# Performance work log

Hardware: AMD Instinct MI355X
Metric: run time of the kernel (lower is better)

Reference implementation:

```python
import jax, jax.numpy as jnp
import numpy as np

N_USERS = 60000
N_ITEMS = 30000
N_NODES = N_USERS + N_ITEMS
D = 64
L = 2


def _norm_adj(edge_index):
    # symmetrize: A_idx = [e, e.flip(0)]
    src = jnp.concatenate([edge_index[0], edge_index[1]])
    dst = jnp.concatenate([edge_index[1], edge_index[0]])
    ones = jnp.ones_like(src, dtype=jnp.float32)
    deg = jax.ops.segment_sum(ones, src, num_segments=N_NODES)
    deg = jnp.clip(deg, 1.0, None)
    val = jax.lax.rsqrt(deg[src]) * jax.lax.rsqrt(deg[dst])
    return src, dst, val


def _spmm(src, dst, val, x):
    # out[i] = sum_{(i,j) in E} val_ij * x[j]
    return jax.ops.segment_sum(val[:, None] * x[dst], src, num_segments=N_NODES)


def setup_inputs() -> dict:
    key = jax.random.key(0)
    ks = jax.random.split(key, 20)
    s = 0.02
    inp = {
        'x_txt': jax.random.normal(ks[0], (N_ITEMS, 768), jnp.float32),
        'x_img': jax.random.normal(ks[1], (N_ITEMS, 512), jnp.float32),
        'x_struct': jax.random.normal(ks[2], (N_ITEMS, 128), jnp.float32),
        'user_emb': jax.random.normal(ks[3], (3, N_USERS, D), jnp.float32) * s,
        'W_txt': jax.random.normal(ks[4], (3, 768, D), jnp.float32) * s,
        'b_txt': jax.random.normal(ks[5], (3, D), jnp.float32) * s,
        'W_img': jax.random.normal(ks[6], (3, 512, D), jnp.float32) * s,
        'b_img': jax.random.normal(ks[7], (3, D), jnp.float32) * s,
        'W_st': jax.random.normal(ks[8], (3, 128, D), jnp.float32) * s,
        'b_st': jax.random.normal(ks[9], (3, D), jnp.float32) * s,
        'Wu1': jax.random.normal(ks[10], (3 * D, 128), jnp.float32) * s,
        'bu1': jax.random.normal(ks[11], (128,), jnp.float32) * s,
        'Wu2': jax.random.normal(ks[12], (128, 3), jnp.float32) * s,
        'bu2': jax.random.normal(ks[13], (3,), jnp.float32) * s,
        'Wi1': jax.random.normal(ks[14], (3 * D, 128), jnp.float32) * s,
        'bi1': jax.random.normal(ks[15], (128,), jnp.float32) * s,
        'Wi2': jax.random.normal(ks[16], (128, 3), jnp.float32) * s,
        'bi2': jax.random.normal(ks[17], (3,), jnp.float32) * s,
        'edge_index': jax.random.randint(ks[18], (2, 500000), 0, N_NODES, jnp.int64),
    }
    return inp


def reference(x_txt, x_img, x_struct, user_emb, W_txt, b_txt, W_img, b_img,
              W_st, b_st, Wu1, bu1, Wu2, bu2, Wi1, bi1, Wi2, bi2, edge_index):
    src, dst, val = _norm_adj(edge_index)

    # item embeddings for all 3 branches at once: [n_items, 3, d]
    i0 = (jnp.einsum('nt,btd->nbd', x_txt, W_txt) + b_txt
          + jnp.einsum('nt,btd->nbd', x_img, W_img) + b_img
          + jnp.einsum('nt,btd->nbd', x_struct, W_st) + b_st)
    u0 = jnp.transpose(user_emb, (1, 0, 2))  # [n_users, 3, d]
    x = jnp.concatenate([u0, i0], axis=0).reshape(N_NODES, 3 * D)

    out = x
    for _ in range(L):
        x = _spmm(src, dst, val, x)
        out = out + x
    out = out / (L + 1)

    stack = out.reshape(N_NODES, 3, D)
    U_stack, I_stack = stack[:N_USERS], stack[N_USERS:]
    U_cat = U_stack.reshape(N_USERS, 3 * D)
    I_cat = I_stack.reshape(N_ITEMS, 3 * D)

    a_u = jax.nn.softmax(jax.nn.relu(U_cat @ Wu1 + bu1) @ Wu2 + bu2, axis=-1)
    a_i = jax.nn.softmax(jax.nn.relu(I_cat @ Wi1 + bi1) @ Wi2 + bi2, axis=-1)

    U = jnp.einsum('nb,nbd->nd', a_u, U_stack)
    I = jnp.einsum('nb,nbd->nd', a_i, I_stack)
    return jnp.concatenate([U, I], axis=0)  # [N_NODES, d]
```

## Files before the change

kernel.cpp:

```cpp
#include <hip/hip_runtime.h>
#include <math.h>

#define N_USERS 60000
#define N_ITEMS 30000
#define N_NODES 90000
#define DD 64
#define FF 192
#define FH 96
#define KK_TOT 1408
#define E_UND 500000
#define E_DIR 1000000
#define SCAN_NBLK 88

typedef __attribute__((ext_vector_type(8))) __bf16 bf16x8;
typedef __attribute__((ext_vector_type(8))) unsigned short u16x8;
typedef __attribute__((ext_vector_type(4))) float f32x4;

__device__ __forceinline__ unsigned short f2bf(float f) {
    unsigned int u = __float_as_uint(f);
    unsigned int r = (u + 0x7FFFu + ((u >> 16) & 1u)) >> 16;
    return (unsigned short)r;
}
__device__ __forceinline__ float bf_lo(unsigned int x) { return __uint_as_float(x << 16); }
__device__ __forceinline__ float bf_hi(unsigned int x) { return __uint_as_float(x & 0xFFFF0000u); }
__device__ __forceinline__ float bf2f(unsigned short x) {
    return __uint_as_float((unsigned int)x << 16);
}
__device__ __forceinline__ unsigned int pack2(float a, float b) {
    return ((unsigned int)f2bf(b) << 16) | (unsigned int)f2bf(a);
}

__global__ void k_mode(const int* __restrict__ ei, int* __restrict__ mode) {
    __shared__ int any;
    if (threadIdx.x == 0) any = 0;
    __syncthreads();
    if (ei[2 * threadIdx.x + 1] != 0) atomicOr(&any, 1);
    __syncthreads();
    if (threadIdx.x == 0) mode[0] = (any == 0) ? 1 : 0;
}

__device__ __forceinline__ void load_pair(const int* __restrict__ ei, int md, int u,
                                          int& a, int& b) {
    if (md) { a = ei[2 * u]; b = ei[2 * (E_UND + u)]; }
    else    { a = ei[u];     b = ei[E_UND + u]; }
}

__global__ void k_deg(const int* __restrict__ ei, const int* __restrict__ mode,
                      int* __restrict__ deg) {
    int i = blockIdx.x * 256 + threadIdx.x;
    if (i >= E_UND) return;
    int md = mode[0];
    int a, b;
    load_pair(ei, md, i, a, b);
    atomicAdd(&deg[a], 1);
    atomicAdd(&deg[b], 1);
}

__global__ __launch_bounds__(1024) void k_scan1(const int* __restrict__ deg,
                                                int* __restrict__ offs,
                                                int* __restrict__ bsum) {
    __shared__ int tmp[1024];
    int b = blockIdx.x, t = threadIdx.x;
    int i = b * 1024 + t;
    int v = (i < N_NODES) ? deg[i] : 0;
    tmp[t] = v;
    __syncthreads();
    for (int off = 1; off < 1024; off <<= 1) {
        int add = (t >= off) ? tmp[t - off] : 0;
        __syncthreads();
        tmp[t] += add;
        __syncthreads();
    }
    offs[i] = tmp[t] - v;
    if (t == 1023) bsum[b] = tmp[t];
}

__global__ void k_scan2(const int* __restrict__ bsum, int* __restrict__ bscan) {
    if (threadIdx.x == 0) {
        int run = 0;
        for (int b = 0; b < SCAN_NBLK; b++) { bscan[b] = run; run += bsum[b]; }
    }
}

__global__ void k_scan3(const int* __restrict__ deg, int* __restrict__ offs,
                        const int* __restrict__ bscan, int* __restrict__ cursor,
                        float* __restrict__ rsq) {
    int i = blockIdx.x * 256 + threadIdx.x;
    if (i >= N_NODES) return;
    int o = offs[i] + bscan[i >> 10];
    offs[i] = o;
    cursor[i] = o;
    int dg = deg[i];
    if (dg < 1) dg = 1;
    rsq[i] = rsqrtf((float)dg);
}

__global__ void k_fill(const int* __restrict__ ei, const int* __restrict__ mode,
                       int* __restrict__ cursor, const float* __restrict__ rsq,
                       int* __restrict__ edst, float* __restrict__ eval) {
    int i = blockIdx.x * 256 + threadIdx.x;
    if (i >= E_DIR) return;
    int md = mode[0];
    int u = (i < E_UND) ? i : i - E_UND;
    int a, b;
    load_pair(ei, md, u, a, b);
    int s, d;
    if (i < E_UND) { s = a; d = b; } else { s = b; d = a; }
    int slot = atomicAdd(&cursor[s], 1);
    edst[slot] = d;
    eval[slot] = rsq[s] * rsq[d];
}

__global__ void k_users(const float* __restrict__ ue, float* __restrict__ S,
                        unsigned short* __restrict__ Xbs) {
    int idx = blockIdx.x * 256 + threadIdx.x;
    if (idx >= N_USERS * FF) return;
    int n = idx / FF;
    int r = idx - n * FF;
    int b = r >> 6, d = r & 63;
    float v = ue[((size_t)b * N_USERS + n) * DD + d];
    S[idx] = v;
    Xbs[idx] = f2bf(v);
}

__global__ void k_cvt_w(const float* __restrict__ Wt, const float* __restrict__ Wi,
                        const float* __restrict__ Wst, unsigned short* __restrict__ Wtb) {
    int idx = blockIdx.x * 256 + threadIdx.x;
    if (idx >= FF * KK_TOT) return;
    int n = idx / KK_TOT;
    int k = idx - n * KK_TOT;
    int b = n >> 6, d = n & 63;
    float v;
    if (k < 768)       v = Wt [((size_t)b * 768 + k) * 64 + d];
    else if (k < 1280) v = Wi [((size_t)b * 512 + (k - 768)) * 64 + d];
    else               v = Wst[((size_t)b * 128 + (k - 1280)) * 64 + d];
    Wtb[idx] = f2bf(v);
}

__global__ void k_cvt_w1(const float* __restrict__ Wu1, const float* __restrict__ Wi1,
                         unsigned short* __restrict__ W1Tu,
                         unsigned short* __restrict__ W1Ti) {
    int idx = blockIdx.x * 256 + threadIdx.x;
    if (idx >= 128 * FF) return;
    int n = idx / FF;
    int k = idx - n * FF;
    W1Tu[idx] = f2bf(Wu1[(size_t)k * 128 + n]);
    W1Ti[idx] = f2bf(Wi1[(size_t)k * 128 + n]);
}

#define BM 128
#define BK 64
#define LDK 72

__global__ __launch_bounds__(256) void k_item_gemm_mfma3(
    const float* __restrict__ xt, const float* __restrict__ xi, const float* __restrict__ xs,
    const unsigned short* __restrict__ Wtb,
    const float* __restrict__ bt, const float* __restrict__ bi, const float* __restrict__ bst,
    float* __restrict__ S, unsigned short* __restrict__ Xbs) {
    __shared__ unsigned short Ash[BM * LDK];
    __shared__ unsigned short Bsh[FF * LDK];
    const int tid  = threadIdx.x;
    const int wave = tid >> 6;
    const int lane = tid & 63;
    const int row0 = blockIdx.x * BM;

    f32x4 acc[2][12];
#pragma unroll
    for (int tm = 0; tm < 2; tm++)
#pragma unroll
        for (int tn = 0; tn < 12; tn++) acc[tm][tn] = (f32x4){0.f, 0.f, 0.f, 0.f};

    for (int k0 = 0; k0 < KK_TOT; k0 += BK) {
#pragma unroll
        for (int i = 0; i < 4; i++) {
            int id = tid + i * 256;
            int r = id >> 3;
            int c = (id & 7) << 3;
            int gr = row0 + r;
            int gk = k0 + c;
            float4 v0 = make_float4(0.f, 0.f, 0.f, 0.f);
            float4 v1 = v0;
            if (gr < N_ITEMS) {
                const float* src;
                int kl;
                if (gk < 768)       { src = xt + (size_t)gr * 768; kl = gk; }
                else if (gk < 1280) { src = xi + (size_t)gr * 512; kl = gk - 768; }
                else                { src = xs + (size_t)gr * 128; kl = gk - 1280; }
                v0 = *(const float4*)(src + kl);
                v1 = *(const float4*)(src + kl + 4);
            }
            u16x8 pk;
            pk[0] = f2bf(v0.x); pk[1] = f2bf(v0.y); pk[2] = f2bf(v0.z); pk[3] = f2bf(v0.w);
            pk[4] = f2bf(v1.x); pk[5] = f2bf(v1.y); pk[6] = f2bf(v1.z); pk[7] = f2bf(v1.w);
            *(u16x8*)(&Ash[r * LDK + c]) = pk;
        }
#pragma unroll
        for (int i = 0; i < 6; i++) {
            int id = tid + i * 256;
            int r = id >> 3;
            int c = (id & 7) << 3;
            *(u16x8*)(&Bsh[r * LDK + c]) =
                *(const u16x8*)(&Wtb[(size_t)r * KK_TOT + k0 + c]);
        }
        __syncthreads();
#pragma unroll
        for (int kk = 0; kk < BK; kk += 32) {
            bf16x8 af[2];
#pragma unroll
            for (int tm = 0; tm < 2; tm++)
                af[tm] = *(const bf16x8*)(&Ash[(wave * 32 + tm * 16 + (lane & 15)) * LDK +
                                               kk + (lane >> 4) * 8]);
#pragma unroll
            for (int tn = 0; tn < 12; tn++) {
                bf16x8 bfr = *(const bf16x8*)(&Bsh[(tn * 16 + (lane & 15)) * LDK +
                                                   kk + (lane >> 4) * 8]);
#pragma unroll
                for (int tm = 0; tm < 2; tm++)
                    acc[tm][tn] = __builtin_amdgcn_mfma_f32_16x16x32_bf16(
                        af[tm], bfr, acc[tm][tn], 0, 0, 0);
            }
        }
        __syncthreads();
    }

    const int col16 = lane & 15;
    const int quad  = lane >> 4;
#pragma unroll
    for (int tn = 0; tn < 12; tn++) {
        int n = tn * 16 + col16;
        int b = n >> 6, d = n & 63;
        float bias = bt[b * 64 + d] + bi[b * 64 + d] + bst[b * 64 + d];
#pragma unroll
        for (int tm = 0; tm < 2; tm++) {
#pragma unroll
            for (int r = 0; r < 4; r++) {
                int row = row0 + wave * 32 + tm * 16 + quad * 4 + r;
                if (row < N_ITEMS) {
                    size_t o = (size_t)(N_USERS + row) * FF + n;
                    float v = acc[tm][tn][r] + bias;
                    S[o] = v;
                    Xbs[o] = f2bf(v);
                }
            }
        }
    }
}

__global__ __launch_bounds__(192) void k_spmm_bf(const unsigned int* __restrict__ Xb,
                                                 unsigned int* __restrict__ Yb,
                                                 float* __restrict__ S,
                                                 const int* __restrict__ offs,
                                                 const int* __restrict__ deg,
                                                 const int* __restrict__ edst,
                                                 const float* __restrict__ eval) {
    int t = threadIdx.x;
    int half = (t >= FH) ? 1 : 0;
    int c = t - half * FH;
    int n = blockIdx.x * 2 + half;
    int start = offs[n];
    int dg = deg[n];
    const int* ed = edst + start;
    const float* ev = eval + start;
    float a0 = 0.f, a1 = 0.f;
    for (int j = 0; j < dg; j += 4) {
        int last = dg - 1;
        int j1 = (j + 1 < dg) ? j + 1 : last;
        int j2 = (j + 2 < dg) ? j + 2 : last;
        int j3 = (j + 3 < dg) ? j + 3 : last;
        int d0 = ed[j], d1 = ed[j1], d2 = ed[j2], d3 = ed[j3];
        float v0 = ev[j];
        float v1 = (j + 1 < dg) ? ev[j1] : 0.f;
        float v2 = (j + 2 < dg) ? ev[j2] : 0.f;
        float v3 = (j + 3 < dg) ? ev[j3] : 0.f;
        unsigned int x0 = Xb[(size_t)d0 * FH + c];
        unsigned int x1 = Xb[(size_t)d1 * FH + c];
        unsigned int x2 = Xb[(size_t)d2 * FH + c];
        unsigned int x3 = Xb[(size_t)d3 * FH + c];
        a0 = fmaf(v0, bf_lo(x0), a0); a1 = fmaf(v0, bf_hi(x0), a1);
        a0 = fmaf(v1, bf_lo(x1), a0); a1 = fmaf(v1, bf_hi(x1), a1);
        a0 = fmaf(v2, bf_lo(x2), a0); a1 = fmaf(v2, bf_hi(x2), a1);
        a0 = fmaf(v3, bf_lo(x3), a0); a1 = fmaf(v3, bf_hi(x3), a1);
    }
    size_t o = (size_t)n * FH + c;
    Yb[o] = pack2(a0, a1);
    float2* Sp = (float2*)(S + (size_t)n * FF);
    float2 s = Sp[c];
    s.x += a0; s.y += a1;
    Sp[c] = s;
}

#define LDA 200

__global__ __launch_bounds__(256) void k_attn_mfma(
    const float* __restrict__ S,
    const unsigned short* __restrict__ W1T,
    const float* __restrict__ B1,
    const float* __restrict__ W2,
    const float* __restrict__ B2,
    float* __restrict__ out,
    int node_base, int n_rows) {
    __shared__ unsigned short Atile[64 * LDA];
    __shared__ float aws[64][4];
    const int tid  = threadIdx.x;
    const int wave = tid >> 6;
    const int lane = tid & 63;
    const int row0 = blockIdx.x * 64;
    const float inv3 = 1.f / 3.f;

#pragma unroll
    for (int i = 0; i < 6; i++) {
        int id = tid + i * 256;
        int r = id / 24;
        int c = (id - r * 24) * 8;
        u16x8 pk;
        if (row0 + r < n_rows) {
            const float* src = S + (size_t)(node_base + row0 + r) * FF + c;
            float4 v0 = *(const float4*)(src);
            float4 v1 = *(const float4*)(src + 4);
            pk[0] = f2bf(v0.x * inv3); pk[1] = f2bf(v0.y * inv3);
            pk[2] = f2bf(v0.z * inv3); pk[3] = f2bf(v0.w * inv3);
            pk[4] = f2bf(v1.x * inv3); pk[5] = f2bf(v1.y * inv3);
            pk[6] = f2bf(v1.z * inv3); pk[7] = f2bf(v1.w * inv3);
        } else {
            pk = (u16x8){0, 0, 0, 0, 0, 0, 0, 0};
        }
        *(u16x8*)(&Atile[r * LDA + c]) = pk;
    }
    __syncthreads();

    f32x4 acc[8];
#pragma unroll
    for (int tn = 0; tn < 8; tn++) acc[tn] = (f32x4){0.f, 0.f, 0.f, 0.f};
    const int l16 = lane & 15;
    const int quad = lane >> 4;
#pragma unroll
    for (int kk = 0; kk < FF; kk += 32) {
        bf16x8 af = *(const bf16x8*)(&Atile[(wave * 16 + l16) * LDA + kk + quad * 8]);
#pragma unroll
        for (int tn = 0; tn < 8; tn++) {
            bf16x8 bf = *(const bf16x8*)(&W1T[(size_t)(tn * 16 + l16) * FF + kk + quad * 8]);
            acc[tn] = __builtin_amdgcn_mfma_f32_16x16x32_bf16(af, bf, acc[tn], 0, 0, 0);
        }
    }

    float pl[4][3];
#pragma unroll
    for (int r = 0; r < 4; r++) { pl[r][0] = 0.f; pl[r][1] = 0.f; pl[r][2] = 0.f; }
#pragma unroll
    for (int tn = 0; tn < 8; tn++) {
        int col = tn * 16 + l16;
        float b1v = B1[col];
        float w0 = W2[col * 3 + 0], w1 = W2[col * 3 + 1], w2v = W2[col * 3 + 2];
#pragma unroll
        for (int r = 0; r < 4; r++) {
            float h = fmaxf(acc[tn][r] + b1v, 0.f);
            pl[r][0] = fmaf(h, w0, pl[r][0]);
            pl[r][1] = fmaf(h, w1, pl[r][1]);
            pl[r][2] = fmaf(h, w2v, pl[r][2]);
        }
    }
#pragma unroll
    for (int m = 1; m <= 8; m <<= 1) {
#pragma unroll
        for (int r = 0; r < 4; r++) {
            pl[r][0] += __shfl_xor(pl[r][0], m, 64);
            pl[r][1] += __shfl_xor(pl[r][1], m, 64);
            pl[r][2] += __shfl_xor(pl[r][2], m, 64);
        }
    }
    float b20 = B2[0], b21 = B2[1], b22 = B2[2];
    if (l16 == 0) {
#pragma unroll
        for (int r = 0; r < 4; r++) {
            float l0 = pl[r][0] + b20, l1 = pl[r][1] + b21, l2 = pl[r][2] + b22;
            float mx = fmaxf(l0, fmaxf(l1, l2));
            float e0 = __expf(l0 - mx), e1 = __expf(l1 - mx), e2 = __expf(l2 - mx);
            float inv = 1.f / (e0 + e1 + e2);
            int rr = wave * 16 + quad * 4 + r;
            aws[rr][0] = e0 * inv; aws[rr][1] = e1 * inv; aws[rr][2] = e2 * inv;
        }
    }
    __syncthreads();

#pragma unroll
    for (int i = 0; i < 16; i++) {
        int flat = tid + i * 256;
        int r = flat >> 6, d = flat & 63;
        if (row0 + r < n_rows) {
            float a0 = aws[r][0], a1 = aws[r][1], a2 = aws[r][2];
            const unsigned short* Ar = &Atile[r * LDA];
            float v = a0 * bf2f(Ar[d]) + a1 * bf2f(Ar[64 + d]) + a2 * bf2f(Ar[128 + d]);
            out[(size_t)(node_base + row0 + r) * DD + d] = v;
        }
    }
}

extern "C" void kernel_launch(void* const* d_in, const int* in_sizes, int n_in,
                              void* d_out, int out_size, void* d_ws, size_t ws_size,
                              hipStream_t stream) {
    (void)in_sizes; (void)n_in; (void)out_size; (void)ws_size;
    const float* x_txt    = (const float*)d_in[0];
    const float* x_img    = (const float*)d_in[1];
    const float* x_struct = (const float*)d_in[2];
    const float* user_emb = (const float*)d_in[3];
    const float* W_txt    = (const float*)d_in[4];
    const float* b_txt    = (const float*)d_in[5];
    const float* W_img    = (const float*)d_in[6];
    const float* b_img    = (const float*)d_in[7];
    const float* W_st     = (const float*)d_in[8];
    const float* b_st     = (const float*)d_in[9];
    const float* Wu1      = (const float*)d_in[10];
    const float* bu1      = (const float*)d_in[11];
    const float* Wu2      = (const float*)d_in[12];
    const float* bu2      = (const float*)d_in[13];
    const float* Wi1      = (const float*)d_in[14];
    const float* bi1      = (const float*)d_in[15];
    const float* Wi2      = (const float*)d_in[16];
    const float* bi2      = (const float*)d_in[17];
    const int*   ei       = (const int*)d_in[18];
    float* out = (float*)d_out;

    char* base = (char*)d_ws;
    size_t off = 0;
    auto take = [&](size_t bytes) -> void* {
        void* p = base + off;
        off += (bytes + 255) & ~(size_t)255;
        return p;
    };
    float* S           = (float*)take((size_t)N_NODES * FF * 4);
    unsigned int* Xb0  = (unsigned int*)take((size_t)N_NODES * FH * 4);
    unsigned int* Yb   = (unsigned int*)take((size_t)N_NODES * FH * 4);
    int* deg    = (int*)take((size_t)N_NODES * 4);
    int* offs   = (int*)take((size_t)SCAN_NBLK * 1024 * 4);
    int* cursor = (int*)take((size_t)N_NODES * 4);
    int* bsum   = (int*)take((size_t)SCAN_NBLK * 4);
    int* bscan  = (int*)take((size_t)SCAN_NBLK * 4);
    float* rsq  = (float*)take((size_t)N_NODES * 4);
    int* edst   = (int*)take((size_t)E_DIR * 4);
    float* eval = (float*)take((size_t)E_DIR * 4);
    int* mode   = (int*)take(256);
    unsigned short* Wtb  = (unsigned short*)take((size_t)FF * KK_TOT * 2);
    unsigned short* W1Tu = (unsigned short*)take((size_t)128 * FF * 2);
    unsigned short* W1Ti = (unsigned short*)take((size_t)128 * FF * 2);

    hipMemsetAsync(deg, 0, (size_t)N_NODES * 4, stream);

    k_mode<<<1, 256, 0, stream>>>(ei, mode);
    k_deg<<<(E_UND + 255) / 256, 256, 0, stream>>>(ei, mode, deg);
    k_scan1<<<SCAN_NBLK, 1024, 0, stream>>>(deg, offs, bsum);
    k_scan2<<<1, 64, 0, stream>>>(bsum, bscan);
    k_scan3<<<(N_NODES + 255) / 256, 256, 0, stream>>>(deg, offs, bscan, cursor, rsq);
    k_fill<<<(E_DIR + 255) / 256, 256, 0, stream>>>(ei, mode, cursor, rsq, edst, eval);

    k_users<<<(N_USERS * FF + 255) / 256, 256, 0, stream>>>(user_emb, S,
                                                            (unsigned short*)Xb0);
    k_cvt_w<<<(FF * KK_TOT + 255) / 256, 256, 0, stream>>>(W_txt, W_img, W_st, Wtb);
    k_cvt_w1<<<(128 * FF + 255) / 256, 256, 0, stream>>>(Wu1, Wi1, W1Tu, W1Ti);
    k_item_gemm_mfma3<<<(N_ITEMS + BM - 1) / BM, 256, 0, stream>>>(
        x_txt, x_img, x_struct, Wtb, b_txt, b_img, b_st, S, (unsigned short*)Xb0);

    k_spmm_bf<<<N_NODES / 2, 192, 0, stream>>>(Xb0, Yb, S, offs, deg, edst, eval);
    k_spmm_bf<<<N_NODES / 2, 192, 0, stream>>>(Yb, Xb0, S, offs, deg, edst, eval);

    k_attn_mfma<<<(N_USERS + 63) / 64, 256, 0, stream>>>(
        S, W1Tu, bu1, Wu2, bu2, out, 0, N_USERS);
    k_attn_mfma<<<(N_ITEMS + 63) / 64, 256, 0, stream>>>(
        S, W1Ti, bi1, Wi2, bi2, out, N_USERS, N_ITEMS);
}
```

Baseline: 697.2 us.

## Split item GEMM into smaller row tiles and two column halves

Reduces the item projection GEMM tile from 128 rows by 192 columns to 64 rows by 96 columns, launching two blocks per row tile, one per half of the output features. This raises the block count well above the CU count and shrinks per-block LDS and accumulator registers, improving occupancy and latency hiding. The trade-off is that each fp32 input row tile is loaded and converted twice, once per column half.

```diff
diff --git a/kernel.cpp b/kernel.cpp
--- a/kernel.cpp
+++ b/kernel.cpp
@@ -148,7 +148,8 @@
     W1Ti[idx] = f2bf(Wi1[(size_t)k * 128 + n]);
 }
 
-#define BM 128
+#define BM 64
+#define BNH 96
 #define BK 64
 #define LDK 72
 
@@ -158,21 +159,23 @@
     const float* __restrict__ bt, const float* __restrict__ bi, const float* __restrict__ bst,
     float* __restrict__ S, unsigned short* __restrict__ Xbs) {
     __shared__ unsigned short Ash[BM * LDK];
-    __shared__ unsigned short Bsh[FF * LDK];
+    __shared__ unsigned short Bsh[BNH * LDK];
     const int tid  = threadIdx.x;
     const int wave = tid >> 6;
     const int lane = tid & 63;
-    const int row0 = blockIdx.x * BM;
-
-    f32x4 acc[2][12];
-#pragma unroll
-    for (int tm = 0; tm < 2; tm++)
-#pragma unroll
-        for (int tn = 0; tn < 12; tn++) acc[tm][tn] = (f32x4){0.f, 0.f, 0.f, 0.f};
+    const int row0 = (blockIdx.x >> 1) * BM;
+    const int n0   = (blockIdx.x & 1) * BNH;
+
+    f32x4 acc[6];
+#pragma unroll
+    for (int tn = 0; tn < 6; tn++) acc[tn] = (f32x4){0.f, 0.f, 0.f, 0.f};
+
+    const int l16  = lane & 15;
+    const int quad = lane >> 4;
 
     for (int k0 = 0; k0 < KK_TOT; k0 += BK) {
 #pragma unroll
-        for (int i = 0; i < 4; i++) {
+        for (int i = 0; i < 2; i++) {
             int id = tid + i * 256;
             int r = id >> 3;
             int c = (id & 7) << 3;
@@ -195,52 +198,39 @@
             *(u16x8*)(&Ash[r * LDK + c]) = pk;
         }
 #pragma unroll
-        for (int i = 0; i < 6; i++) {
+        for (int i = 0; i < 3; i++) {
             int id = tid + i * 256;
             int r = id >> 3;
             int c = (id & 7) << 3;
             *(u16x8*)(&Bsh[r * LDK + c]) =
-                *(const u16x8*)(&Wtb[(size_t)r * KK_TOT + k0 + c]);
+                *(const u16x8*)(&Wtb[(size_t)(n0 + r) * KK_TOT + k0 + c]);
         }
         __syncthreads();
 #pragma unroll
         for (int kk = 0; kk < BK; kk += 32) {
-            bf16x8 af[2];
-#pragma unroll
-            for (int tm = 0; tm < 2; tm++)
-                af[tm] = *(const bf16x8*)(&Ash[(wave * 32 + tm * 16 + (lane & 15)) * LDK +
-                                               kk + (lane >> 4) * 8]);
-#pragma unroll
-            for (int tn = 0; tn < 12; tn++) {
-                bf16x8 bfr = *(const bf16x8*)(&Bsh[(tn * 16 + (lane & 15)) * LDK +
-                                                   kk + (lane >> 4) * 8]);
-#pragma unroll
-                for (int tm = 0; tm < 2; tm++)
-                    acc[tm][tn] = __builtin_amdgcn_mfma_f32_16x16x32_bf16(
-                        af[tm], bfr, acc[tm][tn], 0, 0, 0);
+            bf16x8 af = *(const bf16x8*)(&Ash[(wave * 16 + l16) * LDK + kk + quad * 8]);
+#pragma unroll
+            for (int tn = 0; tn < 6; tn++) {
+                bf16x8 bfr = *(const bf16x8*)(&Bsh[(tn * 16 + l16) * LDK + kk + quad * 8]);
+                acc[tn] = __builtin_amdgcn_mfma_f32_16x16x32_bf16(af, bfr, acc[tn], 0, 0, 0);
             }
         }
         __syncthreads();
     }
 
-    const int col16 = lane & 15;
-    const int quad  = lane >> 4;
-#pragma unroll
-    for (int tn = 0; tn < 12; tn++) {
-        int n = tn * 16 + col16;
+#pragma unroll
+    for (int tn = 0; tn < 6; tn++) {
+        int n = n0 + tn * 16 + l16;
         int b = n >> 6, d = n & 63;
         float bias = bt[b * 64 + d] + bi[b * 64 + d] + bst[b * 64 + d];
 #pragma unroll
-        for (int tm = 0; tm < 2; tm++) {
-#pragma unroll
-            for (int r = 0; r < 4; r++) {
-                int row = row0 + wave * 32 + tm * 16 + quad * 4 + r;
-                if (row < N_ITEMS) {
-                    size_t o = (size_t)(N_USERS + row) * FF + n;
-                    float v = acc[tm][tn][r] + bias;
-                    S[o] = v;
-                    Xbs[o] = f2bf(v);
-                }
+        for (int r = 0; r < 4; r++) {
+            int row = row0 + wave * 16 + quad * 4 + r;
+            if (row < N_ITEMS) {
+                size_t o = (size_t)(N_USERS + row) * FF + n;
+                float v = acc[tn][r] + bias;
+                S[o] = v;
+                Xbs[o] = f2bf(v);
             }
         }
     }
@@ -456,7 +446,7 @@
                                                             (unsigned short*)Xb0);
     k_cvt_w<<<(FF * KK_TOT + 255) / 256, 256, 0, stream>>>(W_txt, W_img, W_st, Wtb);
     k_cvt_w1<<<(128 * FF + 255) / 256, 256, 0, stream>>>(Wu1, Wi1, W1Tu, W1Ti);
-    k_item_gemm_mfma3<<<(N_ITEMS + BM - 1) / BM, 256, 0, stream>>>(
+    k_item_gemm_mfma3<<<((N_ITEMS + BM - 1) / BM) * 2, 256, 0, stream>>>(
         x_txt, x_img, x_struct, Wtb, b_txt, b_img, b_st, S, (unsigned short*)Xb0);
 
     k_spmm_bf<<<N_NODES / 2, 192, 0, stream>>>(Xb0, Yb, S, offs, deg, edst, eval);
```

After: 676.8 us. 1.03x faster.
